# Optimization experiments

Hardware: AMD Instinct MI355X
Metric: run time of the kernel (lower is better)

## Reference

```python
import jax, jax.numpy as jnp
import numpy as np
from jax import lax

# CRF hyperparameters (init_kwargs)
MAX_ITER = 10
POS_W, POS_X_STD, POS_Y_STD = 3.0, 3.0, 3.0
BI_W, BI_X_STD, BI_Y_STD = 10.0, 80.0, 80.0
BI_R_STD, BI_G_STD, BI_B_STD = 13.0, 13.0, 13.0


def setup_inputs() -> dict:
    key = jax.random.key(0)
    k1, k2 = jax.random.split(key)
    U = jax.random.normal(k1, (1, 21, 96, 96), dtype=jnp.float32)      # unary energies
    I = jax.random.uniform(k2, (1, 3, 96, 96), dtype=jnp.float32) * 255.0  # RGB image 0..255
    return {"U": U, "I": I}


def _gauss1d(std):
    r = int(3.0 * std)
    x = jnp.arange(-r, r + 1, dtype=jnp.float32)
    return jnp.exp(-0.5 * (x / std) ** 2), r


def _spatial_raw(x, ky, kx, ry, rx):
    # x: [M, 1, H, W]; unnormalized separable Gaussian filter
    x = lax.conv_general_dilated(x, ky.reshape(1, 1, -1, 1), (1, 1), [(ry, ry), (0, 0)],
                                 dimension_numbers=("NCHW", "OIHW", "NCHW"))
    x = lax.conv_general_dilated(x, kx.reshape(1, 1, 1, -1), (1, 1), [(0, 0), (rx, rx)],
                                 dimension_numbers=("NCHW", "OIHW", "NCHW"))
    return x


def reference(U, I):
    B, L, H, W = U.shape
    N = H * W
    ky, ry = _gauss1d(POS_Y_STD)
    kx, rx = _gauss1d(POS_X_STD)

    # symmetric normalization for the spatial kernel: 1/sqrt(k * 1)
    nsp = lax.rsqrt(_spatial_raw(jnp.ones((1, 1, H, W), jnp.float32), ky, kx, ry, rx))  # [1,1,H,W]

    # bilateral kernel K[b, i, j] = exp(-0.5 ||f_i - f_j||^2) over 5-d features
    yy, xx = jnp.meshgrid(jnp.arange(H, dtype=jnp.float32), jnp.arange(W, dtype=jnp.float32), indexing="ij")
    pos = jnp.stack([xx.ravel() / BI_X_STD, yy.ravel() / BI_Y_STD], axis=-1)  # [N, 2]
    rgb_std = jnp.array([BI_R_STD, BI_G_STD, BI_B_STD], jnp.float32)
    col = I.reshape(B, 3, N).transpose(0, 2, 1) / rgb_std                     # [B, N, 3]
    feats = jnp.concatenate([jnp.broadcast_to(pos[None], (B, N, 2)), col], axis=-1)  # [B, N, 5]
    sq = jnp.sum(feats * feats, axis=-1)                                      # [B, N]
    D = sq[:, :, None] + sq[:, None, :] - 2.0 * jnp.einsum("bnf,bmf->bnm", feats, feats)
    K = jnp.exp(-0.5 * jnp.maximum(D, 0.0))                                   # [B, N, N]
    nbi = lax.rsqrt(jnp.sum(K, axis=-1, keepdims=True))                       # [B, N, 1]

    Q0 = jax.nn.softmax(-U, axis=1)

    def step(Q, _):
        Qf = Q.reshape(B * L, 1, H, W)
        sp_msg = POS_W * (nsp * _spatial_raw(nsp * Qf, ky, kx, ry, rx)).reshape(B, L, H, W)
        Qflat = Q.transpose(0, 2, 3, 1).reshape(B, N, L)
        bi = nbi * jnp.einsum("bnm,bml->bnl", K, nbi * Qflat)
        bi_msg = BI_W * bi.reshape(B, H, W, L).transpose(0, 3, 1, 2)
        # Potts compatibility (negative identity): agreeing mass raises the logit
        Qn = jax.nn.softmax(-U + sp_msg + bi_msg, axis=1)
        return Qn, None

    Q, _ = lax.scan(step, Q0, None, length=MAX_ITER)
    return Q
```

## Files before the change

### kernel.cpp

```cpp
#include <hip/hip_runtime.h>
#include <hip/hip_bf16.h>
#include <stddef.h>

#define HH 96
#define WW 96
#define NPIX 9216
#define LBL 21
#define LPAD 32
#define RAD 9
#define N_ITER 10
#define POS_W_C 3.0f
#define BI_W_C 10.0f
#define INV_XY (1.0f/80.0f)
#define INV_RGB (1.0f/13.0f)

#define JCH 16
#define JC (NPIX / JCH)
#define JTOT (NPIX / 32)
#define ROWB (JC * 2 + 16)
#define CHROW (ROWB / 16)
#define TOTCH (32 * CHROW)
#define ITILE 128
#define NITB (NPIX / ITILE)
#define NSPB (LBL * 24)
#define KSPLIT 4
#define PSTR 24

typedef __bf16 bf16x8 __attribute__((ext_vector_type(8)));
typedef float  f32x4  __attribute__((ext_vector_type(4)));

__device__ const float GK[2 * RAD + 1] = {
    0.01110900f, 0.02856548f, 0.06572886f, 0.13533528f, 0.24935220f,
    0.41111229f, 0.60653066f, 0.80073740f, 0.94595947f, 1.00000000f,
    0.94595947f, 0.80073740f, 0.60653066f, 0.41111229f, 0.24935220f,
    0.13533528f, 0.06572886f, 0.02856548f, 0.01110900f
};

__device__ __forceinline__ unsigned short f2bf(float f) {
    unsigned u = __float_as_uint(f);
    unsigned r = (u + 0x7fffu + ((u >> 16) & 1u)) >> 16;
    return (unsigned short)r;
}
__device__ __forceinline__ float bf2f(unsigned short s) {
    return __uint_as_float(((unsigned)s) << 16);
}
__device__ __forceinline__ unsigned pk2bf(float a, float b) {
    __hip_bfloat162 h = __float22bfloat162_rn(make_float2(a, b));
    return *(unsigned*)&h;
}

__global__ void k_prep(const float* __restrict__ I,
                       float* __restrict__ fx, float* __restrict__ fy,
                       float* __restrict__ fr, float* __restrict__ fg,
                       float* __restrict__ fb, float* __restrict__ S,
                       float* __restrict__ nsp) {
    int n = blockIdx.x * 256 + threadIdx.x;
    if (n >= NPIX) return;
    int y = n / WW, x = n % WW;
    float vx = (float)x * INV_XY;
    float vy = (float)y * INV_XY;
    float vr = I[n] * INV_RGB;
    float vg = I[NPIX + n] * INV_RGB;
    float vb = I[2 * NPIX + n] * INV_RGB;
    fx[n] = vx; fy[n] = vy; fr[n] = vr; fg[n] = vg; fb[n] = vb;
    S[n] = -0.5f * (vx*vx + vy*vy + vr*vr + vg*vg + vb*vb);
    float sy = 0.f, sx = 0.f;
    #pragma unroll
    for (int d = -RAD; d <= RAD; ++d) {
        float g = GK[d + RAD];
        if ((unsigned)(y + d) < HH) sy += g;
        if ((unsigned)(x + d) < WW) sx += g;
    }
    nsp[n] = rsqrtf(sy * sx);
}

template <bool STORE>
__global__ void __launch_bounds__(256)
k_K(const float* __restrict__ fx, const float* __restrict__ fy,
    const float* __restrict__ fr, const float* __restrict__ fg,
    const float* __restrict__ fb, const float* __restrict__ S,
    float* __restrict__ RS, unsigned short* __restrict__ K) {
    int it = blockIdx.x >> 2;
    int part = blockIdx.x & 3;
    int tid = threadIdx.x;
    int m = tid & 15;
    int g = tid >> 4;
    int khs = g & 3;
    int ts = g >> 2;
    int i = it * 16 + m;
    float hx = fx[i], hy = fy[i], hr = fr[i], hg = fg[i], hb = fb[i];
    float ci = S[i];
    unsigned short* Kb = K + (size_t)it * JTOT * 512;
    float sum = 0.f;
    for (int pass = 0; pass < JTOT / (4 * KSPLIT); ++pass) {
        int jtile = part * (JTOT / KSPLIT) + pass * 4 + ts;
        int j = jtile * 32 + khs * 8;
        float4 x0 = *(const float4*)(fx + j), x1 = *(const float4*)(fx + j + 4);
        float4 y0 = *(const float4*)(fy + j), y1 = *(const float4*)(fy + j + 4);
        float4 r0 = *(const float4*)(fr + j), r1 = *(const float4*)(fr + j + 4);
        float4 g0 = *(const float4*)(fg + j), g1 = *(const float4*)(fg + j + 4);
        float4 b0 = *(const float4*)(fb + j), b1 = *(const float4*)(fb + j + 4);
        float4 s0 = *(const float4*)(S + j),  s1 = *(const float4*)(S + j + 4);
        float k0 = __expf(ci + s0.x + hx*x0.x + hy*y0.x + hr*r0.x + hg*g0.x + hb*b0.x);
        float k1 = __expf(ci + s0.y + hx*x0.y + hy*y0.y + hr*r0.y + hg*g0.y + hb*b0.y);
        float k2 = __expf(ci + s0.z + hx*x0.z + hy*y0.z + hr*r0.z + hg*g0.z + hb*b0.z);
        float k3 = __expf(ci + s0.w + hx*x0.w + hy*y0.w + hr*r0.w + hg*g0.w + hb*b0.w);
        float k4 = __expf(ci + s1.x + hx*x1.x + hy*y1.x + hr*r1.x + hg*g1.x + hb*b1.x);
        float k5 = __expf(ci + s1.y + hx*x1.y + hy*y1.y + hr*r1.y + hg*g1.y + hb*b1.y);
        float k6 = __expf(ci + s1.z + hx*x1.z + hy*y1.z + hr*r1.z + hg*g1.z + hb*b1.z);
        float k7 = __expf(ci + s1.w + hx*x1.w + hy*y1.w + hr*r1.w + hg*g1.w + hb*b1.w);
        sum += ((k0 + k1) + (k2 + k3)) + ((k4 + k5) + (k6 + k7));
        if (STORE) {
            uint4 u;
            u.x = pk2bf(k0, k1);
            u.y = pk2bf(k2, k3);
            u.z = pk2bf(k4, k5);
            u.w = pk2bf(k6, k7);
            *(uint4*)(Kb + (size_t)jtile * 512 + (tid & 63) * 8) = u;
        }
    }
    __shared__ float red[16][17];
    red[g][m] = sum;
    __syncthreads();
    if (tid < 16) {
        float tot = 0.f;
        #pragma unroll
        for (int q = 0; q < 16; ++q) tot += red[q][tid];
        RS[part * NPIX + it * 16 + tid] = tot;
    }
}

__global__ void k_q0(const float* __restrict__ U, const float* __restrict__ RS,
                     const float* __restrict__ nsp,
                     float* __restrict__ nbi, float* __restrict__ A,
                     unsigned short* __restrict__ Qt0, unsigned short* __restrict__ Qt1) {
    int n = blockIdx.x * 256 + threadIdx.x;
    if (n >= NPIX) return;
    float nb = rsqrtf(RS[n] + RS[NPIX + n] + RS[2 * NPIX + n] + RS[3 * NPIX + n]);
    nbi[n] = nb;
    float v[LBL];
    float mx = -1e30f;
    #pragma unroll
    for (int l = 0; l < LBL; ++l) { v[l] = -U[l * NPIX + n]; mx = fmaxf(mx, v[l]); }
    float s = 0.f;
    #pragma unroll
    for (int l = 0; l < LBL; ++l) { v[l] = __expf(v[l] - mx); s += v[l]; }
    float inv = 1.f / s;
    float ns = nsp[n];
    #pragma unroll
    for (int l = 0; l < LBL; ++l) {
        float q = v[l] * inv;
        A[l * NPIX + n] = ns * q;
        Qt0[l * NPIX + n] = f2bf(nb * q);
    }
    #pragma unroll
    for (int l = LBL; l < LPAD; ++l) { Qt0[l * NPIX + n] = 0; Qt1[l * NPIX + n] = 0; }
}

__global__ void k_sp(const float* __restrict__ A, const float* __restrict__ nsp,
                     const float* __restrict__ U, float* __restrict__ SP) {
    __shared__ float ty[4 * WW];
    int l = blockIdx.x / 24;
    int y0 = (blockIdx.x % 24) * 4;
    int t = threadIdx.x;
    const float* Al = A + (size_t)l * NPIX;
    #pragma unroll
    for (int c = 0; c < 2; ++c) {
        int p = t + c * 256;
        if (p < 4 * WW) {
            int yy = p / WW, x = p % WW;
            int y = y0 + yy;
            float s = 0.f;
            #pragma unroll
            for (int d = -RAD; d <= RAD; ++d) {
                int yd = y + d;
                if ((unsigned)yd < HH) s += GK[d + RAD] * Al[yd * WW + x];
            }
            ty[p] = s;
        }
    }
    __syncthreads();
    #pragma unroll
    for (int c = 0; c < 2; ++c) {
        int p = t + c * 256;
        if (p < 4 * WW) {
            int yy = p / WW, x = p % WW;
            float s = 0.f;
            #pragma unroll
            for (int d = -RAD; d <= RAD; ++d) {
                int xd = x + d;
                if ((unsigned)xd < WW) s += GK[d + RAD] * ty[yy * WW + xd];
            }
            int pp = (y0 + yy) * WW + x;
            SP[(size_t)l * NPIX + pp] = POS_W_C * nsp[pp] * s - U[(size_t)l * NPIX + pp];
        }
    }
}

__global__ void __launch_bounds__(256)
k_bi_fast(const unsigned short* __restrict__ K, const unsigned short* __restrict__ Qt,
          const float* __restrict__ A, const float* __restrict__ nsp,
          const float* __restrict__ U, float* __restrict__ SP,
          float* __restrict__ P) {
    __shared__ __align__(16) unsigned short Bsh[32 * ROWB / 2];
    int tid = threadIdx.x;
    int bid = blockIdx.x;

    if (bid < NSPB) {
        float* ty = (float*)Bsh;
        int l = bid / 24;
        int y0b = (bid % 24) * 4;
        const float* Al = A + (size_t)l * NPIX;
        #pragma unroll
        for (int c = 0; c < 2; ++c) {
            int p = tid + c * 256;
            if (p < 4 * WW) {
                int yy = p / WW, x = p % WW;
                int y = y0b + yy;
                float s = 0.f;
                #pragma unroll
                for (int d = -RAD; d <= RAD; ++d) {
                    int yd = y + d;
                    if ((unsigned)yd < HH) s += GK[d + RAD] * Al[yd * WW + x];
                }
                ty[p] = s;
            }
        }
        __syncthreads();
        #pragma unroll
        for (int c = 0; c < 2; ++c) {
            int p = tid + c * 256;
            if (p < 4 * WW) {
                int yy = p / WW, x = p % WW;
                float s = 0.f;
                #pragma unroll
                for (int d = -RAD; d <= RAD; ++d) {
                    int xd = x + d;
                    if ((unsigned)xd < WW) s += GK[d + RAD] * ty[yy * WW + xd];
                }
                int pp = (y0b + yy) * WW + x;
                SP[(size_t)l * NPIX + pp] = POS_W_C * nsp[pp] * s - U[(size_t)l * NPIX + pp];
            }
        }
        __syncthreads();
    }

    int jc  = bid / NITB;
    int itb = bid % NITB;
    int base_j = jc * JC;
    int jtb = jc * (JC / 32);

    for (int itn = 0; itn < (TOTCH + 255) / 256; ++itn) {
        int c = itn * 256 + tid;
        if (c < TOTCH) {
            int l = c / CHROW;
            int off = c - l * CHROW;
            int off16 = (off == CHROW - 1) ? 0 : off;
            uint4 v = *(const uint4*)(Qt + (size_t)l * NPIX + base_j + off16 * 8);
            *((uint4*)Bsh + c) = v;
        }
    }
    __syncthreads();

    int lane = tid & 63;
    int wv = tid >> 6;
    int m  = lane & 15;
    int kh = lane >> 4;

    const bf16x8* pa0 = (const bf16x8*)K + ((size_t)(itb * 8 + wv)     * JTOT + jtb) * 64 + lane;
    const bf16x8* pa1 = (const bf16x8*)K + ((size_t)(itb * 8 + 4 + wv) * JTOT + jtb) * 64 + lane;
    const char* lb0 = (const char*)Bsh + m * ROWB + kh * 16;
    const char* lb1 = (const char*)Bsh + (m + 16) * ROWB + kh * 16;

    f32x4 acc00 = {0.f,0.f,0.f,0.f}, acc01 = {0.f,0.f,0.f,0.f};
    f32x4 acc10 = {0.f,0.f,0.f,0.f}, acc11 = {0.f,0.f,0.f,0.f};

    #pragma unroll 6
    for (int jt = 0; jt < JC / 32; ++jt) {
        bf16x8 a0 = pa0[jt * 64];
        bf16x8 a1 = pa1[jt * 64];
        bf16x8 b0 = *(const bf16x8*)(lb0 + jt * 64);
        bf16x8 b1 = *(const bf16x8*)(lb1 + jt * 64);
        acc00 = __builtin_amdgcn_mfma_f32_16x16x32_bf16(a0, b0, acc00, 0, 0, 0);
        acc01 = __builtin_amdgcn_mfma_f32_16x16x32_bf16(a0, b1, acc01, 0, 0, 0);
        acc10 = __builtin_amdgcn_mfma_f32_16x16x32_bf16(a1, b0, acc10, 0, 0, 0);
        acc11 = __builtin_amdgcn_mfma_f32_16x16x32_bf16(a1, b1, acc11, 0, 0, 0);
    }

    float* Pp = P + (size_t)jc * NPIX * PSTR;
    int i0 = itb * 128 + wv * 16 + kh * 4;
    int i1 = i0 + 64;
    #pragma unroll
    for (int r = 0; r < 4; ++r) {
        Pp[(size_t)(i0 + r) * PSTR + m] = acc00[r];
        Pp[(size_t)(i1 + r) * PSTR + m] = acc10[r];
        if (m < 8) {
            Pp[(size_t)(i0 + r) * PSTR + 16 + m] = acc01[r];
            Pp[(size_t)(i1 + r) * PSTR + 16 + m] = acc11[r];
        }
    }
}

__global__ void __launch_bounds__(64)
k_red(const float* __restrict__ P, const float* __restrict__ SP,
      const float* __restrict__ nbi, const float* __restrict__ nsp,
      float* __restrict__ Qo, float* __restrict__ Ao,
      unsigned short* __restrict__ Qto) {
    int lane = threadIdx.x;
    int p = blockIdx.x * 32 + (lane & 31);
    int h = lane >> 5;
    float4 s[6] = {{0,0,0,0},{0,0,0,0},{0,0,0,0},{0,0,0,0},{0,0,0,0},{0,0,0,0}};
    #pragma unroll
    for (int jj = 0; jj < JCH / 2; ++jj) {
        int jcc = h * (JCH / 2) + jj;
        const float4* pp = (const float4*)(P + ((size_t)jcc * NPIX + p) * PSTR);
        #pragma unroll
        for (int q = 0; q < 6; ++q) s[q] += pp[q];
    }
    float bi[24];
    #pragma unroll
    for (int q = 0; q < 6; ++q) {
        bi[4*q+0] = s[q].x + __shfl_down(s[q].x, 32);
        bi[4*q+1] = s[q].y + __shfl_down(s[q].y, 32);
        bi[4*q+2] = s[q].z + __shfl_down(s[q].z, 32);
        bi[4*q+3] = s[q].w + __shfl_down(s[q].w, 32);
    }
    if (h) return;

    float nb = nbi[p];
    float ns = nsp[p];
    float v[LBL];
    float mx = -1e30f;
    #pragma unroll
    for (int l = 0; l < LBL; ++l) {
        v[l] = SP[l * NPIX + p] + BI_W_C * nb * bi[l];
        mx = fmaxf(mx, v[l]);
    }
    float ssum = 0.f;
    #pragma unroll
    for (int l = 0; l < LBL; ++l) { v[l] = __expf(v[l] - mx); ssum += v[l]; }
    float inv = 1.f / ssum;
    #pragma unroll
    for (int l = 0; l < LBL; ++l) {
        float q = v[l] * inv;
        Qo[l * NPIX + p] = q;
        Ao[l * NPIX + p] = ns * q;
        Qto[l * NPIX + p] = f2bf(nb * q);
    }
}

__global__ void k_bi_slow(const float* __restrict__ fx, const float* __restrict__ fy,
                          const float* __restrict__ fr, const float* __restrict__ fg,
                          const float* __restrict__ fb,
                          const float* __restrict__ nbi, const unsigned short* __restrict__ Qt,
                          const float* __restrict__ SP, const float* __restrict__ nsp,
                          float* __restrict__ Qo, float* __restrict__ Ao,
                          unsigned short* __restrict__ Qto) {
    int t = threadIdx.x;
    int px = t & 15, st = t >> 4;
    int i = blockIdx.x * 16 + px;
    float xi = fx[i], yi = fy[i], ri = fr[i], gi = fg[i], bi = fb[i];
    float acc[LBL];
    #pragma unroll
    for (int l = 0; l < LBL; ++l) acc[l] = 0.f;
    int j0 = st * (NPIX / 16);
    for (int j = j0; j < j0 + NPIX / 16; ++j) {
        float dx = xi - fx[j], dy = yi - fy[j];
        float dr = ri - fr[j], dg = gi - fg[j], db = bi - fb[j];
        float D = dx*dx + dy*dy + dr*dr + dg*dg + db*db;
        float w = __expf(-0.5f * D);
        #pragma unroll
        for (int l = 0; l < LBL; ++l) acc[l] += w * bf2f(Qt[l * NPIX + j]);
    }
    __shared__ float red[16][LBL];
    if (st == 0) {
        #pragma unroll
        for (int l = 0; l < LBL; ++l) red[px][l] = acc[l];
    }
    __syncthreads();
    for (int s = 1; s < 16; ++s) {
        if (st == s) {
            #pragma unroll
            for (int l = 0; l < LBL; ++l) red[px][l] += acc[l];
        }
        __syncthreads();
    }
    if (t < 16) {
        int i2 = blockIdx.x * 16 + t;
        float nb = nbi[i2];
        float ns = nsp[i2];
        float v[LBL];
        float mx = -1e30f;
        #pragma unroll
        for (int l = 0; l < LBL; ++l) {
            v[l] = SP[l * NPIX + i2] + BI_W_C * nb * red[t][l];
            mx = fmaxf(mx, v[l]);
        }
        float s = 0.f;
        #pragma unroll
        for (int l = 0; l < LBL; ++l) { v[l] = __expf(v[l] - mx); s += v[l]; }
        float inv = 1.f / s;
        #pragma unroll
        for (int l = 0; l < LBL; ++l) {
            float q = v[l] * inv;
            Qo[l * NPIX + i2] = q;
            Ao[l * NPIX + i2] = ns * q;
            Qto[l * NPIX + i2] = f2bf(nb * q);
        }
    }
}

extern "C" void kernel_launch(void* const* d_in, const int* in_sizes, int n_in,
                              void* d_out, int out_size, void* d_ws, size_t ws_size,
                              hipStream_t stream) {
    const float* U = (const float*)d_in[0];
    const float* I = (const float*)d_in[1];

    char* w = (char*)d_ws;
    float* fx  = (float*)w;                 w += NPIX * sizeof(float);
    float* fy  = (float*)w;                 w += NPIX * sizeof(float);
    float* fr  = (float*)w;                 w += NPIX * sizeof(float);
    float* fg  = (float*)w;                 w += NPIX * sizeof(float);
    float* fb  = (float*)w;                 w += NPIX * sizeof(float);
    float* S   = (float*)w;                 w += NPIX * sizeof(float);
    float* nsp = (float*)w;                 w += NPIX * sizeof(float);
    float* nbi = (float*)w;                 w += NPIX * sizeof(float);
    float* RS  = (float*)w;                 w += (size_t)KSPLIT * NPIX * sizeof(float);
    float* A   = (float*)w;                 w += (size_t)LBL * NPIX * sizeof(float);
    float* SP  = (float*)w;                 w += (size_t)LBL * NPIX * sizeof(float);
    unsigned short* Qtb[2];
    Qtb[0] = (unsigned short*)w;            w += (size_t)LPAD * NPIX * sizeof(unsigned short);
    Qtb[1] = (unsigned short*)w;            w += (size_t)LPAD * NPIX * sizeof(unsigned short);
    float* P = (float*)w;                   w += (size_t)JCH * NPIX * PSTR * sizeof(float);
    unsigned short* K = (unsigned short*)w;
    size_t need = (size_t)(w - (char*)d_ws) + (size_t)NPIX * NPIX * sizeof(unsigned short);
    bool fast = (ws_size >= need);

    float* Qout = (float*)d_out;

    k_prep<<<(NPIX + 255) / 256, 256, 0, stream>>>(I, fx, fy, fr, fg, fb, S, nsp);
    if (fast) k_K<true ><<<(NPIX / 16) * KSPLIT, 256, 0, stream>>>(fx, fy, fr, fg, fb, S, RS, K);
    else      k_K<false><<<(NPIX / 16) * KSPLIT, 256, 0, stream>>>(fx, fy, fr, fg, fb, S, RS, nullptr);
    k_q0<<<(NPIX + 255) / 256, 256, 0, stream>>>(U, RS, nsp, nbi, A, Qtb[0], Qtb[1]);

    for (int t = 0; t < N_ITER; ++t) {
        const unsigned short* Qtin = Qtb[t & 1];
        unsigned short* Qtout = Qtb[(t + 1) & 1];
        if (fast) {
            k_bi_fast<<<NITB * JCH, 256, 0, stream>>>(K, Qtin, A, nsp, U, SP, P);
            k_red<<<NPIX / 32, 64, 0, stream>>>(P, SP, nbi, nsp, Qout, A, Qtout);
        } else {
            k_sp<<<NSPB, 256, 0, stream>>>(A, nsp, U, SP);
            k_bi_slow<<<NPIX / 16, 256, 0, stream>>>(fx, fy, fr, fg, fb, nbi, Qtin, SP, nsp, Qout, A, Qtout);
        }
    }
}
```

Before: 520.7 us.

## Store Q in MFMA-fragment layout and read B operands directly from global

Rewrites the Q transpose buffer into a layout that matches the MFMA B-fragment order, so k_bi_fast loads B operands straight from global memory with coalesced 16-byte reads instead of staging them through shared memory with a sync. The I tile per block is halved (one 16-row MFMA tile per wave) to raise block count and occupancy, and launch bounds ask for 8 blocks per CU. The K-build split is doubled, and k_red now uses 256 threads with a shared-memory reduction across 8 groups instead of two half-waves. This trades B-operand reuse from LDS for repeated global or L2 reads of Q across waves.

```diff
diff --git a/kernel.cpp b/kernel.cpp
--- a/kernel.cpp
+++ b/kernel.cpp
@@ -17,14 +17,12 @@
 #define JCH 16
 #define JC (NPIX / JCH)
 #define JTOT (NPIX / 32)
-#define ROWB (JC * 2 + 16)
-#define CHROW (ROWB / 16)
-#define TOTCH (32 * CHROW)
-#define ITILE 128
+#define ITILE 64
 #define NITB (NPIX / ITILE)
 #define NSPB (LBL * 24)
-#define KSPLIT 4
+#define KSPLIT 8
 #define PSTR 24
+#define QHALF (JTOT * 64 * 8)
 
 typedef __bf16 bf16x8 __attribute__((ext_vector_type(8)));
 typedef float  f32x4  __attribute__((ext_vector_type(4)));
@@ -47,6 +45,10 @@
 __device__ __forceinline__ unsigned pk2bf(float a, float b) {
     __hip_bfloat162 h = __float22bfloat162_rn(make_float2(a, b));
     return *(unsigned*)&h;
+}
+__device__ __forceinline__ size_t qtidx(int p, int l) {
+    size_t half = (l >> 4) ? (size_t)QHALF : 0;
+    return half + ((((p >> 5) * 64 + ((p >> 3) & 3) * 16 + (l & 15)) << 3) + (p & 7));
 }
 
 __global__ void k_prep(const float* __restrict__ I,
@@ -80,8 +82,8 @@
     const float* __restrict__ fr, const float* __restrict__ fg,
     const float* __restrict__ fb, const float* __restrict__ S,
     float* __restrict__ RS, unsigned short* __restrict__ K) {
-    int it = blockIdx.x >> 2;
-    int part = blockIdx.x & 3;
+    int it = blockIdx.x >> 3;
+    int part = blockIdx.x & 7;
     int tid = threadIdx.x;
     int m = tid & 15;
     int g = tid >> 4;
@@ -136,7 +138,10 @@
                      unsigned short* __restrict__ Qt0, unsigned short* __restrict__ Qt1) {
     int n = blockIdx.x * 256 + threadIdx.x;
     if (n >= NPIX) return;
-    float nb = rsqrtf(RS[n] + RS[NPIX + n] + RS[2 * NPIX + n] + RS[3 * NPIX + n]);
+    float rs = 0.f;
+    #pragma unroll
+    for (int q = 0; q < KSPLIT; ++q) rs += RS[q * NPIX + n];
+    float nb = rsqrtf(rs);
     nbi[n] = nb;
     float v[LBL];
     float mx = -1e30f;
@@ -151,10 +156,13 @@
     for (int l = 0; l < LBL; ++l) {
         float q = v[l] * inv;
         A[l * NPIX + n] = ns * q;
-        Qt0[l * NPIX + n] = f2bf(nb * q);
-    }
-    #pragma unroll
-    for (int l = LBL; l < LPAD; ++l) { Qt0[l * NPIX + n] = 0; Qt1[l * NPIX + n] = 0; }
+        Qt0[qtidx(n, l)] = f2bf(nb * q);
+    }
+    #pragma unroll
+    for (int l = LBL; l < LPAD; ++l) {
+        Qt0[qtidx(n, l)] = 0;
+        Qt1[qtidx(n, l)] = 0;
+    }
 }
 
 __global__ void k_sp(const float* __restrict__ A, const float* __restrict__ nsp,
@@ -197,17 +205,16 @@
     }
 }
 
-__global__ void __launch_bounds__(256)
+__global__ void __launch_bounds__(256, 8)
 k_bi_fast(const unsigned short* __restrict__ K, const unsigned short* __restrict__ Qt,
           const float* __restrict__ A, const float* __restrict__ nsp,
           const float* __restrict__ U, float* __restrict__ SP,
           float* __restrict__ P) {
-    __shared__ __align__(16) unsigned short Bsh[32 * ROWB / 2];
     int tid = threadIdx.x;
     int bid = blockIdx.x;
 
+    __shared__ float ty[4 * WW];
     if (bid < NSPB) {
-        float* ty = (float*)Bsh;
         int l = bid / 24;
         int y0b = (bid % 24) * 4;
         const float* Al = A + (size_t)l * NPIX;
@@ -242,90 +249,70 @@
                 SP[(size_t)l * NPIX + pp] = POS_W_C * nsp[pp] * s - U[(size_t)l * NPIX + pp];
             }
         }
-        __syncthreads();
     }
 
     int jc  = bid / NITB;
     int itb = bid % NITB;
-    int base_j = jc * JC;
     int jtb = jc * (JC / 32);
-
-    for (int itn = 0; itn < (TOTCH + 255) / 256; ++itn) {
-        int c = itn * 256 + tid;
-        if (c < TOTCH) {
-            int l = c / CHROW;
-            int off = c - l * CHROW;
-            int off16 = (off == CHROW - 1) ? 0 : off;
-            uint4 v = *(const uint4*)(Qt + (size_t)l * NPIX + base_j + off16 * 8);
-            *((uint4*)Bsh + c) = v;
-        }
-    }
-    __syncthreads();
 
     int lane = tid & 63;
     int wv = tid >> 6;
     int m  = lane & 15;
     int kh = lane >> 4;
-
-    const bf16x8* pa0 = (const bf16x8*)K + ((size_t)(itb * 8 + wv)     * JTOT + jtb) * 64 + lane;
-    const bf16x8* pa1 = (const bf16x8*)K + ((size_t)(itb * 8 + 4 + wv) * JTOT + jtb) * 64 + lane;
-    const char* lb0 = (const char*)Bsh + m * ROWB + kh * 16;
-    const char* lb1 = (const char*)Bsh + (m + 16) * ROWB + kh * 16;
-
-    f32x4 acc00 = {0.f,0.f,0.f,0.f}, acc01 = {0.f,0.f,0.f,0.f};
-    f32x4 acc10 = {0.f,0.f,0.f,0.f}, acc11 = {0.f,0.f,0.f,0.f};
+    int it = itb * 4 + wv;
+
+    const bf16x8* pa  = (const bf16x8*)K  + ((size_t)it * JTOT + jtb) * 64 + lane;
+    const bf16x8* pb0 = (const bf16x8*)Qt + (size_t)jtb * 64 + lane;
+    const bf16x8* pb1 = (const bf16x8*)Qt + (size_t)(QHALF / 8) + (size_t)jtb * 64 + lane;
+
+    f32x4 acc0 = {0.f,0.f,0.f,0.f}, acc1 = {0.f,0.f,0.f,0.f};
 
     #pragma unroll 6
     for (int jt = 0; jt < JC / 32; ++jt) {
-        bf16x8 a0 = pa0[jt * 64];
-        bf16x8 a1 = pa1[jt * 64];
-        bf16x8 b0 = *(const bf16x8*)(lb0 + jt * 64);
-        bf16x8 b1 = *(const bf16x8*)(lb1 + jt * 64);
-        acc00 = __builtin_amdgcn_mfma_f32_16x16x32_bf16(a0, b0, acc00, 0, 0, 0);
-        acc01 = __builtin_amdgcn_mfma_f32_16x16x32_bf16(a0, b1, acc01, 0, 0, 0);
-        acc10 = __builtin_amdgcn_mfma_f32_16x16x32_bf16(a1, b0, acc10, 0, 0, 0);
-        acc11 = __builtin_amdgcn_mfma_f32_16x16x32_bf16(a1, b1, acc11, 0, 0, 0);
+        bf16x8 a  = pa[jt * 64];
+        bf16x8 b0 = pb0[jt * 64];
+        bf16x8 b1 = pb1[jt * 64];
+        acc0 = __builtin_amdgcn_mfma_f32_16x16x32_bf16(a, b0, acc0, 0, 0, 0);
+        acc1 = __builtin_amdgcn_mfma_f32_16x16x32_bf16(a, b1, acc1, 0, 0, 0);
     }
 
     float* Pp = P + (size_t)jc * NPIX * PSTR;
-    int i0 = itb * 128 + wv * 16 + kh * 4;
-    int i1 = i0 + 64;
+    int i0 = it * 16 + kh * 4;
     #pragma unroll
     for (int r = 0; r < 4; ++r) {
-        Pp[(size_t)(i0 + r) * PSTR + m] = acc00[r];
-        Pp[(size_t)(i1 + r) * PSTR + m] = acc10[r];
-        if (m < 8) {
-            Pp[(size_t)(i0 + r) * PSTR + 16 + m] = acc01[r];
-            Pp[(size_t)(i1 + r) * PSTR + 16 + m] = acc11[r];
-        }
-    }
-}
-
-__global__ void __launch_bounds__(64)
+        Pp[(size_t)(i0 + r) * PSTR + m] = acc0[r];
+        if (m < 8) Pp[(size_t)(i0 + r) * PSTR + 16 + m] = acc1[r];
+    }
+}
+
+__global__ void __launch_bounds__(256)
 k_red(const float* __restrict__ P, const float* __restrict__ SP,
       const float* __restrict__ nbi, const float* __restrict__ nsp,
       float* __restrict__ Qo, float* __restrict__ Ao,
       unsigned short* __restrict__ Qto) {
-    int lane = threadIdx.x;
-    int p = blockIdx.x * 32 + (lane & 31);
-    int h = lane >> 5;
+    __shared__ float red[8][32][25];
+    int tid = threadIdx.x;
+    int p32 = tid & 31;
+    int g = tid >> 5;
+    int p = blockIdx.x * 32 + p32;
+
     float4 s[6] = {{0,0,0,0},{0,0,0,0},{0,0,0,0},{0,0,0,0},{0,0,0,0},{0,0,0,0}};
     #pragma unroll
-    for (int jj = 0; jj < JCH / 2; ++jj) {
-        int jcc = h * (JCH / 2) + jj;
+    for (int jj = 0; jj < 2; ++jj) {
+        int jcc = g * 2 + jj;
         const float4* pp = (const float4*)(P + ((size_t)jcc * NPIX + p) * PSTR);
         #pragma unroll
         for (int q = 0; q < 6; ++q) s[q] += pp[q];
     }
-    float bi[24];
     #pragma unroll
     for (int q = 0; q < 6; ++q) {
-        bi[4*q+0] = s[q].x + __shfl_down(s[q].x, 32);
-        bi[4*q+1] = s[q].y + __shfl_down(s[q].y, 32);
-        bi[4*q+2] = s[q].z + __shfl_down(s[q].z, 32);
-        bi[4*q+3] = s[q].w + __shfl_down(s[q].w, 32);
-    }
-    if (h) return;
+        red[g][p32][4*q+0] = s[q].x;
+        red[g][p32][4*q+1] = s[q].y;
+        red[g][p32][4*q+2] = s[q].z;
+        red[g][p32][4*q+3] = s[q].w;
+    }
+    __syncthreads();
+    if (tid >= 32) return;
 
     float nb = nbi[p];
     float ns = nsp[p];
@@ -333,7 +320,10 @@
     float mx = -1e30f;
     #pragma unroll
     for (int l = 0; l < LBL; ++l) {
-        v[l] = SP[l * NPIX + p] + BI_W_C * nb * bi[l];
+        float bi = 0.f;
+        #pragma unroll
+        for (int q = 0; q < 8; ++q) bi += red[q][p32][l];
+        v[l] = SP[l * NPIX + p] + BI_W_C * nb * bi;
         mx = fmaxf(mx, v[l]);
     }
     float ssum = 0.f;
@@ -345,7 +335,7 @@
         float q = v[l] * inv;
         Qo[l * NPIX + p] = q;
         Ao[l * NPIX + p] = ns * q;
-        Qto[l * NPIX + p] = f2bf(nb * q);
+        Qto[qtidx(p, l)] = f2bf(nb * q);
     }
 }
 
@@ -370,7 +360,7 @@
         float D = dx*dx + dy*dy + dr*dr + dg*dg + db*db;
         float w = __expf(-0.5f * D);
         #pragma unroll
-        for (int l = 0; l < LBL; ++l) acc[l] += w * bf2f(Qt[l * NPIX + j]);
+        for (int l = 0; l < LBL; ++l) acc[l] += w * bf2f(Qt[qtidx(j, l)]);
     }
     __shared__ float red[16][LBL];
     if (st == 0) {
@@ -405,7 +395,7 @@
             float q = v[l] * inv;
             Qo[l * NPIX + i2] = q;
             Ao[l * NPIX + i2] = ns * q;
-            Qto[l * NPIX + i2] = f2bf(nb * q);
+            Qto[qtidx(i2, l)] = f2bf(nb * q);
         }
     }
 }
@@ -429,8 +419,8 @@
     float* A   = (float*)w;                 w += (size_t)LBL * NPIX * sizeof(float);
     float* SP  = (float*)w;                 w += (size_t)LBL * NPIX * sizeof(float);
     unsigned short* Qtb[2];
-    Qtb[0] = (unsigned short*)w;            w += (size_t)LPAD * NPIX * sizeof(unsigned short);
-    Qtb[1] = (unsigned short*)w;            w += (size_t)LPAD * NPIX * sizeof(unsigned short);
+    Qtb[0] = (unsigned short*)w;            w += (size_t)2 * QHALF * sizeof(unsigned short);
+    Qtb[1] = (unsigned short*)w;            w += (size_t)2 * QHALF * sizeof(unsigned short);
     float* P = (float*)w;                   w += (size_t)JCH * NPIX * PSTR * sizeof(float);
     unsigned short* K = (unsigned short*)w;
     size_t need = (size_t)(w - (char*)d_ws) + (size_t)NPIX * NPIX * sizeof(unsigned short);
@@ -448,7 +438,7 @@
         unsigned short* Qtout = Qtb[(t + 1) & 1];
         if (fast) {
             k_bi_fast<<<NITB * JCH, 256, 0, stream>>>(K, Qtin, A, nsp, U, SP, P);
-            k_red<<<NPIX / 32, 64, 0, stream>>>(P, SP, nbi, nsp, Qout, A, Qtout);
+            k_red<<<NPIX / 32, 256, 0, stream>>>(P, SP, nbi, nsp, Qout, A, Qtout);
         } else {
             k_sp<<<NSPB, 256, 0, stream>>>(A, nsp, U, SP);
             k_bi_slow<<<NPIX / 16, 256, 0, stream>>>(fx, fy, fr, fg, fb, nbi, Qtin, SP, nsp, Qout, A, Qtout);
```

New measurement: 509.4 us. 2.2% less time.
